# Kernel optimization log

Hardware: AMD Instinct MI355X
Metric: run time of the kernel (lower is better)

The kernel has to match this reference:

```python
import jax, jax.numpy as jnp
import numpy as np

# (a1,a2,a3,a4,b1,b2,b3,b4,xi_E,xi_I,mu,e,k) per oscillator type
PARAMS = {
    1: (0.0, 5.0, 5.0, 1.0, 0.0, -1.0, 1.0, 0.0, 0.0, 0.0, 5.0, 0.001, 500),
    2: (0.5, 0.55, 0.55, -0.5, 0.5, -0.55, -0.55, -0.5, 0.0, 0.0, 1.0, 0.001, 50),
    3: (0.5, 0.6, 0.55, 0.5, -0.5, -0.6, -0.55, 0.5, 0.0, 0.0, 1.0, 0.001, 50),
    4: (-0.5, 0.55, 0.55, -0.5, -0.5, -0.55, -0.55, 0.5, 0.0, 0.0, 1.0, 0.001, 50),
    5: (-0.9, 0.9, 0.9, -0.9, 0.9, -0.9, -0.9, 0.9, 0.0, 0.0, 1.0, 0.001, 50),
    6: (-0.9, 0.9, 0.9, -0.9, 0.9, -0.9, -0.9, 0.9, 0.0, 0.0, 1.0, 0.001, 300),
    7: (-5.0, 5.0, 5.0, -5.0, 1.0, -1.0, -1.0, 1.0, 0.0, 0.0, 1.0, 0.001, 50),
    8: (-5.0, 5.0, 5.0, -5.0, 1.0, -1.0, -1.0, 1.0, 0.0, 0.0, 1.0, 0.001, 300),
}
N_STEPS = 100  # torch runs t = 0..99 producing LORS[1..100], then max over those


def _lee_forward(x, osc_type):
    a1, a2, a3, a4, b1, b2, b3, b4, xi_E, xi_I, mu, e, k = PARAMS[osc_type]
    # stimulus with tiny sign-dependent offset; constant over time
    sim0 = x + e * jnp.sign(x)
    damp = jnp.exp(-k * sim0 * sim0)   # exp(-k*sim0^2), constant over time
    omega = jnp.tanh(mu * sim0)        # Omega[t+1] is the same every step
    E0 = jnp.full_like(x, 0.2)
    I0 = jnp.zeros_like(x)
    L0 = jnp.full_like(x, 0.2)
    m0 = jnp.full_like(x, -jnp.inf)    # running max over LORS[1..100]

    def step(carry, _):
        E, I, L, m = carry
        E1 = jnp.tanh(mu * (a1 * L + a2 * E - a3 * I + a4 * sim0 - xi_E))
        I1 = jnp.tanh(mu * (b1 * L - b2 * E - b3 * I + b4 * sim0 - xi_I))
        L1 = (E1 - I1) * damp + omega
        return (E1, I1, L1, jnp.maximum(m, L1)), None

    (_, _, _, m), _ = jax.lax.scan(step, (E0, I0, L0, m0), None, length=N_STEPS)
    return m


def setup_inputs() -> dict:
    key = jax.random.key(0)
    x = jax.random.normal(key, (2048, 512), dtype=jnp.float32)
    return {"x": x, "oscillator_type": 1}


def reference(x, oscillator_type):
    # output shape == x.shape: time-max-pooled LORS activation
    return _lee_forward(x, oscillator_type)
```

## Files before the change

kernel.cpp:

```cpp
#include <hip/hip_runtime.h>
#include <math.h>


#define N_STEPS 100

typedef float v2f __attribute__((ext_vector_type(2)));
__device__ __forceinline__ v2f splat2(float s){ v2f v; v.x = s; v.y = s; return v; }

__constant__ float PAR[8][13] = {
    { 0.0f,  5.0f,  5.0f,  1.0f,  0.0f, -1.0f,  1.0f,  0.0f, 0.0f, 0.0f, 5.0f, 0.001f, 500.0f},
    { 0.5f,  0.55f, 0.55f, -0.5f,  0.5f, -0.55f, -0.55f, -0.5f, 0.0f, 0.0f, 1.0f, 0.001f, 50.0f},
    { 0.5f,  0.6f,  0.55f,  0.5f, -0.5f, -0.6f,  -0.55f,  0.5f, 0.0f, 0.0f, 1.0f, 0.001f, 50.0f},
    {-0.5f,  0.55f, 0.55f, -0.5f, -0.5f, -0.55f, -0.55f,  0.5f, 0.0f, 0.0f, 1.0f, 0.001f, 50.0f},
    {-0.9f,  0.9f,  0.9f,  -0.9f,  0.9f, -0.9f,  -0.9f,   0.9f, 0.0f, 0.0f, 1.0f, 0.001f, 50.0f},
    {-0.9f,  0.9f,  0.9f,  -0.9f,  0.9f, -0.9f,  -0.9f,   0.9f, 0.0f, 0.0f, 1.0f, 0.001f, 300.0f},
    {-5.0f,  5.0f,  5.0f,  -5.0f,  1.0f, -1.0f,  -1.0f,   1.0f, 0.0f, 0.0f, 1.0f, 0.001f, 50.0f},
    {-5.0f,  5.0f,  5.0f,  -5.0f,  1.0f, -1.0f,  -1.0f,   1.0f, 0.0f, 0.0f, 1.0f, 0.001f, 300.0f},
};

__device__ __forceinline__ float xla_tanhf(float x) {
#pragma clang fp contract(off)
    float ax = fabsf(x);
    float xc = fminf(fmaxf(x, -7.99881172180175781f), 7.99881172180175781f);
    float x2 = xc * xc;
    float p = -2.76076847742355e-16f;
    p = fmaf(p, x2, 2.00018790482477e-13f);
    p = fmaf(p, x2, -8.60467152213735e-11f);
    p = fmaf(p, x2, 5.12229709037114e-08f);
    p = fmaf(p, x2, 1.48572235717979e-05f);
    p = fmaf(p, x2, 6.37261928875436e-04f);
    p = fmaf(p, x2, 4.89352455891786e-03f);
    float num = xc * p;
    float q = 1.19825839466702e-06f;
    q = fmaf(q, x2, 1.18534705686654e-04f);
    q = fmaf(q, x2, 2.26843463243900e-03f);
    q = fmaf(q, x2, 4.89352518554385e-03f);
    float r = num / q;
    return (ax < 0.0004f) ? x : r;
}

__device__ __forceinline__ v2f xla_tanh2(v2f x) {
#pragma clang fp contract(off)
    const float C = 7.99881172180175781f;
    v2f xc = __builtin_elementwise_min(__builtin_elementwise_max(x, splat2(-C)), splat2(C));
    v2f x2 = xc * xc;
    v2f p = splat2(-2.76076847742355e-16f);
    p = __builtin_elementwise_fma(p, x2, splat2(2.00018790482477e-13f));
    p = __builtin_elementwise_fma(p, x2, splat2(-8.60467152213735e-11f));
    p = __builtin_elementwise_fma(p, x2, splat2(5.12229709037114e-08f));
    p = __builtin_elementwise_fma(p, x2, splat2(1.48572235717979e-05f));
    p = __builtin_elementwise_fma(p, x2, splat2(6.37261928875436e-04f));
    p = __builtin_elementwise_fma(p, x2, splat2(4.89352455891786e-03f));
    v2f num = xc * p;
    v2f q = splat2(1.19825839466702e-06f);
    q = __builtin_elementwise_fma(q, x2, splat2(1.18534705686654e-04f));
    q = __builtin_elementwise_fma(q, x2, splat2(2.26843463243900e-03f));
    q = __builtin_elementwise_fma(q, x2, splat2(4.89352518554385e-03f));
    float rE = num.x / q.x;
    float rI = num.y / q.y;
    v2f r;
    r.x = (fabsf(x.x) < 0.0004f) ? x.x : rE;
    r.y = (fabsf(x.y) < 0.0004f) ? x.y : rI;
    return r;
}

__device__ __forceinline__ float xla_expf(float x) {
#pragma clang fp contract(off)
    float xc = fminf(fmaxf(x, -88.3762626647949f), 88.3762626647950f);
    float fx = floorf(fmaf(xc, 1.44269504088896341f, 0.5f));
    float r = fmaf(fx, -0.693359375f, xc);
    r = fmaf(fx, 2.12194440e-4f, r);
    float r2 = r * r;
    float y = 1.9875691500e-4f;
    y = fmaf(y, r, 1.3981999507e-3f);
    y = fmaf(y, r, 8.3334519073e-3f);
    y = fmaf(y, r, 4.1665795894e-2f);
    y = fmaf(y, r, 1.6666665459e-1f);
    y = fmaf(y, r, 5.0000001201e-1f);
    y = fmaf(y, r2, r);
    y = y + 1.0f;
    int n2 = (int)fx;
    float p2n = __int_as_float((n2 + 127) << 23);
    return y * p2n;
}

__device__ __forceinline__ void preamble(float xv, const float* p,
                                         float& sim0, float& damp, float& omega) {
#pragma clang fp contract(off)
    float mu = p[10], e = p[11], k = p[12];
    float sgn  = (xv > 0.0f) ? 1.0f : ((xv < 0.0f) ? -1.0f : 0.0f);
    sim0 = fmaf(e, sgn, xv);
    float targ = (-k * sim0) * sim0;
    damp  = xla_expf(targ);
    omega = xla_tanhf(mu * sim0);
}

__device__ __forceinline__ bool fast_omega(float damp, float omega) {
    return (2.0f * damp) < (fabsf(omega) * 0x1p-26f);
}

__device__ __forceinline__ bool slow_t1(float xv, float e) {
#pragma clang fp contract(off)
    float sgn  = (xv > 0.0f) ? 1.0f : ((xv < 0.0f) ? -1.0f : 0.0f);
    float sim0 = fmaf(e, sgn, xv);
    return fabsf(sim0) <= 0.21f;
}

__device__ __forceinline__ float loop_t1(float sim0, float damp, float omega) {
#pragma clang fp contract(off)
    float E = 0.2f, I = 0.0f;
    float Dmax = -INFINITY;
    for (int s = 0; s < N_STEPS; ++s) {
        float tE = 5.0f * E;
        v2f mulc; mulc.x = -5.0f; mulc.y = -1.0f;
        v2f iv   = splat2(I);
        v2f addv; addv.x = tE;    addv.y = E;
        v2f u = __builtin_elementwise_fma(mulc, iv, addv);
        float sE = u.x + sim0;
        v2f pre; pre.x = sE; pre.y = u.y;
        v2f args = splat2(5.0f) * pre;
        v2f t = xla_tanh2(args);
        float D = t.x - t.y;
        Dmax = fmaxf(Dmax, D);
        E = t.x; I = t.y;
    }
    return fmaf(Dmax, damp, omega);
}

__device__ __forceinline__ float loop_gen(const float* p, float sim0,
                                          float damp, float omega) {
#pragma clang fp contract(off)
    float a1 = p[0], a2 = p[1], a3 = p[2], a4 = p[3];
    float b1 = p[4], b2 = p[5], b3 = p[6], b4 = p[7];
    float xiE = p[8], xiI = p[9], mu = p[10];
    float nb2 = -b2;
    float E = 0.2f, I = 0.0f, L = 0.2f;
    float m = -INFINITY;
    for (int s = 0; s < N_STEPS; ++s) {
        float tE = a2 * E;
        float uE = fmaf(a1, L, tE);
        uE = fmaf(-a3, I, uE);
        uE = fmaf(a4, sim0, uE);
        uE = uE - xiE;
        float argE = mu * uE;
        float tI = nb2 * E;
        float uI = fmaf(b1, L, tI);
        uI = fmaf(-b3, I, uI);
        uI = fmaf(b4, sim0, uI);
        uI = uI - xiI;
        float argI = mu * uI;
        float E1 = xla_tanhf(argE);
        float I1 = xla_tanhf(argI);
        float d = E1 - I1;
        L = fmaf(d, damp, omega);
        E = E1; I = I1;
        m = fmaxf(m, L);
    }
    return m;
}

__device__ __forceinline__ bool classify_slow(float xv, int t, const float* p) {
    if (t == 1) return slow_t1(xv, p[11]);
    float sim0, damp, omega;
    preamble(xv, p, sim0, damp, omega);
    return !fast_omega(damp, omega);
}


__global__ __launch_bounds__(256)
void k_count(const float* __restrict__ x, const int* __restrict__ osc_type,
             unsigned* __restrict__ bcount, int n)
{
    __shared__ unsigned wc[4];
    int i = blockIdx.x * 256 + threadIdx.x;
    int t = *osc_type;
    const float* p = PAR[t - 1];
    bool slow = (i < n) && classify_slow(x[i], t, p);
    unsigned long long mask = __ballot(slow);
    int lane = threadIdx.x & 63, wid = threadIdx.x >> 6;
    if (lane == 0) wc[wid] = (unsigned)__popcll(mask);
    __syncthreads();
    if (threadIdx.x == 0) bcount[blockIdx.x] = wc[0] + wc[1] + wc[2] + wc[3];
}

__global__ __launch_bounds__(256)
void k_fill(const float* __restrict__ x, const int* __restrict__ osc_type,
            float* __restrict__ out, unsigned* __restrict__ bcount,
            unsigned* __restrict__ wl, int n, int NB)
{
#pragma clang fp contract(off)
    __shared__ unsigned sums[256];
    __shared__ unsigned woff[4];
    int tid = threadIdx.x;
    int bid = blockIdx.x;

    unsigned s = 0;
    for (int j = tid; j < bid; j += 256) s += bcount[j];
    sums[tid] = s;
    __syncthreads();
    for (int off = 128; off > 0; off >>= 1) {
        if (tid < off) sums[tid] += sums[tid + off];
        __syncthreads();
    }
    unsigned bbase = sums[0];

    int i = bid * 256 + tid;
    bool active = (i < n);
    int t = *osc_type;
    const float* p = PAR[t - 1];
    float xv = active ? x[i] : 1.0e9f;
    bool slow = active && classify_slow(xv, t, p);
    if (active && !slow) {
        float mu = p[10], e = p[11];
        float sgn  = (xv > 0.0f) ? 1.0f : ((xv < 0.0f) ? -1.0f : 0.0f);
        float sim0 = fmaf(e, sgn, xv);
        out[i] = xla_tanhf(mu * sim0);
    }
    unsigned long long mask = __ballot(slow);
    int lane = tid & 63, wid = tid >> 6;
    if (lane == 0) woff[wid] = (unsigned)__popcll(mask);
    __syncthreads();
    if (slow) {
        unsigned base = bbase;
        for (int w = 0; w < wid; ++w) base += woff[w];
        base += (unsigned)__popcll(mask & ((1ull << lane) - 1ull));
        wl[base] = (unsigned)i;
    }
    if (tid == 0 && bid == NB - 1)
        bcount[NB] = bbase + woff[0] + woff[1] + woff[2] + woff[3];
}

__global__ __launch_bounds__(64)
void k_process(const float* __restrict__ x, const int* __restrict__ osc_type,
               float* __restrict__ out, const unsigned* __restrict__ total_p,
               const unsigned* __restrict__ wl)
{
#pragma clang fp contract(off)
    unsigned total = *total_p;
    int t = *osc_type;
    const float* p = PAR[t - 1];
    unsigned stride = gridDim.x * 64u;
    for (unsigned tid = blockIdx.x * 64u + threadIdx.x; tid < total; tid += stride) {
        int i = (int)wl[tid];
        float sim0, damp, omega;
        preamble(x[i], p, sim0, damp, omega);
        out[i] = (t == 1) ? loop_t1(sim0, damp, omega)
                          : loop_gen(p, sim0, damp, omega);
    }
}

__global__ __launch_bounds__(256)
void k_monolithic(const float* __restrict__ x, const int* __restrict__ osc_type,
                  float* __restrict__ out, int n)
{
#pragma clang fp contract(off)
    int i = blockIdx.x * 256 + threadIdx.x;
    if (i >= n) return;
    int t = *osc_type;
    const float* p = PAR[t - 1];
    float sim0, damp, omega;
    preamble(x[i], p, sim0, damp, omega);
    if (fast_omega(damp, omega)) { out[i] = omega; return; }
    out[i] = (t == 1) ? loop_t1(sim0, damp, omega)
                      : loop_gen(p, sim0, damp, omega);
}

extern "C" void kernel_launch(void* const* d_in, const int* in_sizes, int n_in,
                              void* d_out, int out_size, void* d_ws, size_t ws_size,
                              hipStream_t stream) {
    const float* x        = (const float*)d_in[0];
    const int*   osc_type = (const int*)d_in[1];
    float*       out      = (float*)d_out;
    int n = in_sizes[0];
    int NB = (n + 255) / 256;

    size_t needed = ((size_t)NB + 1 + (size_t)n) * sizeof(unsigned);
    if (ws_size >= needed) {
        unsigned* bcount = (unsigned*)d_ws;
        unsigned* wl     = bcount + NB + 1;
        k_count  <<<NB, 256, 0, stream>>>(x, osc_type, bcount, n);
        k_fill   <<<NB, 256, 0, stream>>>(x, osc_type, out, bcount, wl, n, NB);
        k_process<<<4096, 64, 0, stream>>>(x, osc_type, out, bcount + NB, wl);
    } else {
        k_monolithic<<<NB, 256, 0, stream>>>(x, osc_type, out, n);
    }
}
```

Before: 48.86 us.

## Split type-1 E/I tanh pair across adjacent lanes using DPP swap

For oscillator type 1, each slow element is now handled by two adjacent lanes. One lane computes the E tanh and the other the I tanh, and the results are exchanged each step with a DPP quad-permute, so the serial dependency chain per step holds one tanh instead of two. The running max is taken on E1-I1 and damp/omega are applied once at the end, relying on damp being non-negative. Blocks grow to 128 threads to keep the same number of work items per block, at the cost of doubling the lanes spent per element.

```diff
diff --git a/kernel.cpp b/kernel.cpp
--- a/kernel.cpp
+++ b/kernel.cpp
@@ -230,7 +230,7 @@
         bcount[NB] = bbase + woff[0] + woff[1] + woff[2] + woff[3];
 }
 
-__global__ __launch_bounds__(64)
+__global__ __launch_bounds__(128)
 void k_process(const float* __restrict__ x, const int* __restrict__ osc_type,
                float* __restrict__ out, const unsigned* __restrict__ total_p,
                const unsigned* __restrict__ wl)
@@ -239,13 +239,45 @@
     unsigned total = *total_p;
     int t = *osc_type;
     const float* p = PAR[t - 1];
-    unsigned stride = gridDim.x * 64u;
-    for (unsigned tid = blockIdx.x * 64u + threadIdx.x; tid < total; tid += stride) {
-        int i = (int)wl[tid];
-        float sim0, damp, omega;
-        preamble(x[i], p, sim0, damp, omega);
-        out[i] = (t == 1) ? loop_t1(sim0, damp, omega)
-                          : loop_gen(p, sim0, damp, omega);
+    if (t == 1) {
+        bool odd = (threadIdx.x & 1u) != 0u;
+        unsigned pairIdx = (blockIdx.x * 128u + threadIdx.x) >> 1;
+        unsigned pstride = gridDim.x * 64u;
+        for (; pairIdx < total; pairIdx += pstride) {
+            int i = (int)wl[pairIdx];
+            float sim0, damp, omega;
+            preamble(x[i], p, sim0, damp, omega);
+            float E = 0.2f, I = 0.0f;
+            float Dmax = -INFINITY;
+            for (int s = 0; s < N_STEPS; ++s) {
+                float tE = 5.0f * E;
+                float uE = fmaf(-5.0f, I, tE);
+                float sE = uE + sim0;
+                float aE = 5.0f * sE;
+                float vI = E - I;
+                float aI = 5.0f * vI;
+                float arg = odd ? aI : aE;
+                float tn  = xla_tanhf(arg);
+                int   pi  = __builtin_amdgcn_mov_dpp(__float_as_int(tn),
+                                                     0xB1, 0xF, 0xF, true);
+                float tp  = __int_as_float(pi);
+                float E1 = odd ? tp : tn;
+                float I1 = odd ? tn : tp;
+                float D  = E1 - I1;
+                Dmax = fmaxf(Dmax, D);
+                E = E1; I = I1;
+            }
+            if (!odd) out[i] = fmaf(Dmax, damp, omega);
+        }
+    } else {
+        unsigned tid = blockIdx.x * 128u + threadIdx.x;
+        unsigned stride = gridDim.x * 128u;
+        for (; tid < total; tid += stride) {
+            int i = (int)wl[tid];
+            float sim0, damp, omega;
+            preamble(x[i], p, sim0, damp, omega);
+            out[i] = loop_gen(p, sim0, damp, omega);
+        }
     }
 }
 
@@ -280,7 +312,7 @@
         unsigned* wl     = bcount + NB + 1;
         k_count  <<<NB, 256, 0, stream>>>(x, osc_type, bcount, n);
         k_fill   <<<NB, 256, 0, stream>>>(x, osc_type, out, bcount, wl, n, NB);
-        k_process<<<4096, 64, 0, stream>>>(x, osc_type, out, bcount + NB, wl);
+        k_process<<<4096, 128, 0, stream>>>(x, osc_type, out, bcount + NB, wl);
     } else {
         k_monolithic<<<NB, 256, 0, stream>>>(x, osc_type, out, n);
     }
```

After: 55.74 us. +14.1%, slower.
